# Optimization experiments

Hardware: AMD Instinct MI355X
Metric: run time of the kernel (lower is better)

The kernel has to match this reference:

```python
import jax, jax.numpy as jnp
import numpy as np

N_LEVELS = 16  # 3**16 = 43_046_721


def setup_inputs() -> dict:
    key = jax.random.key(0)
    k1, k2 = jax.random.split(key)
    f = jax.random.normal(k1, (3 ** N_LEVELS,), dtype=jnp.float32)
    # torch.rand -> uniform [0, 1)
    Phi_P = jax.random.uniform(k2, (N_LEVELS, 3, 3), dtype=jnp.float32)
    return {"f": f, "Phi_P": Phi_P}


def reference(f, Phi_P):
    N = Phi_P.shape[0]
    # Row-orthonormalize each 3x3 block: QR of Phi_P^T, then take Q^T
    Q, _ = jnp.linalg.qr(jnp.swapaxes(Phi_P, -2, -1))  # batched reduced QR
    Phi = jnp.swapaxes(Q, -2, -1)  # [N, 3, 3], orthonormal rows

    # Recursive Haar-style butterfly. At level i, f has length 3**(N-i).
    # Detail coefficients (rows j=1,2) land in slots [3**(N-i-1), 3**(N-i));
    # the row-0 (average) branch recurses. Build segments and concatenate
    # in reverse to avoid scatter into a preallocated buffer.
    segs = []
    for i in range(N):
        fm = f.reshape(-1, 3)            # [3**(N-i-1), 3]
        d1 = fm @ Phi[i, 1, :]           # detail j=1
        d2 = fm @ Phi[i, 2, :]           # detail j=2
        segs.append(jnp.concatenate([d1, d2]))
        f = fm @ Phi[i, 0, :]            # average branch, length /3
    # f now has length 1; its single entry is f_hat[0]
    f_hat = jnp.concatenate([f[:1]] + segs[::-1])
    return f_hat
```

## Files before the change

### kernel.cpp

```cpp
#include <hip/hip_runtime.h>

#define TPB 256

typedef float f32x4 __attribute__((ext_vector_type(4)));

__device__ __forceinline__ void block_sync_lds() {
    asm volatile("s_waitcnt lgkmcnt(0)" ::: "memory");
    __builtin_amdgcn_s_barrier();
    asm volatile("" ::: "memory");
}

__device__ __forceinline__ float sgpr(float x) {
    return __int_as_float(__builtin_amdgcn_readfirstlane(__float_as_int(x)));
}

__device__ __forceinline__ void gload_lds16(const float* g, float* l) {
    __builtin_amdgcn_global_load_lds(
        (const __attribute__((address_space(1))) void*)g,
        (__attribute__((address_space(3))) void*)l, 16, 0, 0);
}
__device__ __forceinline__ void gload_lds4(const float* g, float* l) {
    __builtin_amdgcn_global_load_lds(
        (const __attribute__((address_space(1))) void*)g,
        (__attribute__((address_space(3))) void*)l, 4, 0, 0);
}

__device__ __forceinline__ void qr3(const float* __restrict__ M, float* __restrict__ P) {
    float A[3][3];
#pragma unroll
    for (int r = 0; r < 3; ++r)
#pragma unroll
        for (int c = 0; c < 3; ++c)
            A[r][c] = M[c * 3 + r];

    float V[3][3], tau[3];
#pragma unroll
    for (int k = 0; k < 3; ++k) {
        float alpha = A[k][k];
        float xn2 = 0.f;
#pragma unroll
        for (int r = k + 1; r < 3; ++r) xn2 += A[r][k] * A[r][k];
        float t = 0.f;
        float v[3] = {0.f, 0.f, 0.f};
        v[k] = 1.f;
        if (xn2 > 0.f) {
            float beta = -copysignf(sqrtf(alpha * alpha + xn2), alpha);
            t = (beta - alpha) / beta;
            float inv = 1.f / (alpha - beta);
#pragma unroll
            for (int r = k + 1; r < 3; ++r) v[r] = A[r][k] * inv;
#pragma unroll
            for (int c = 0; c < 3; ++c) {
                if (c < k) continue;
                float w = 0.f;
#pragma unroll
                for (int r = 0; r < 3; ++r) if (r >= k) w += v[r] * A[r][c];
                w *= t;
#pragma unroll
                for (int r = 0; r < 3; ++r) if (r >= k) A[r][c] -= w * v[r];
            }
        }
        tau[k] = t;
#pragma unroll
        for (int r = 0; r < 3; ++r) V[k][r] = v[r];
    }
    float Q[3][3] = {{1.f, 0.f, 0.f}, {0.f, 1.f, 0.f}, {0.f, 0.f, 1.f}};
#pragma unroll
    for (int k = 2; k >= 0; --k) {
#pragma unroll
        for (int c = 0; c < 3; ++c) {
            float w = 0.f;
#pragma unroll
            for (int r = 0; r < 3; ++r) w += V[k][r] * Q[r][c];
            w *= tau[k];
#pragma unroll
            for (int r = 0; r < 3; ++r) Q[r][c] -= w * V[k][r];
        }
    }
#pragma unroll
    for (int r = 0; r < 3; ++r)
#pragma unroll
        for (int c = 0; c < 3; ++c)
            P[r * 3 + c] = Q[c][r];
}

#define ORG_D1L0 0
#define ORG_D2L0 1160
#define ORG_D1L1 2320
#define ORG_D2L1 2712
#define ORG_D1L2 3104
#define ORG_D2L2 3240

__global__ __launch_bounds__(TPB, 8) void fused3_kernel(
        const float* __restrict__ in, float* __restrict__ out,
        float* __restrict__ avg_out, const float* __restrict__ PhiP,
        int lvl, int m2) {
    __shared__ float s[3456];
    const int  t = threadIdx.x;
    const long b = blockIdx.x;
    const long nF = 27L * m2;
    const long fBase = 3456L * b;
    const long M0 = 9L * m2, M1 = 3L * m2, M2 = m2;

    const bool full = (128L * (b + 1) <= (long)m2);

    const long A0 = M0 + 1152L * b;
    const long A1 = 2 * M0 + 1152L * b;
    const long A2 = M1 + 384L * b;
    const long A3 = 2 * M1 + 384L * b;
    const long A4 = M2 + 128L * b;
    const long A5 = 2 * M2 + 128L * b;
    const int o0 = (int)(A0 & 3), o1 = (int)(A1 & 3), o2 = (int)(A2 & 3);
    const int o3 = (int)(A3 & 3), o4 = (int)(A4 & 3), o5 = (int)(A5 & 3);

    if (full) {
        const float* src = in + fBase;
#pragma unroll
        for (int r = 0; r < 3; ++r) {
            int c = 256 * r + t;
            gload_lds16(src + 4 * c, &s[4 * c]);
        }
        {
            int c = 608 + t;
            gload_lds16(src + 4 * c, &s[4 * c]);
        }
    } else {
        const long rem = nF - fBase;
        for (int i = t; i < 3456; i += TPB) s[i] = (i < rem) ? in[fBase + i] : 0.f;
    }

    float P[27];
    qr3(PhiP + 9L * lvl,       P + 0);
    qr3(PhiP + 9L * (lvl + 1), P + 9);
    qr3(PhiP + 9L * (lvl + 2), P + 18);
#pragma unroll
    for (int j = 0; j < 27; ++j) P[j] = sgpr(P[j]);

    __syncthreads();

    float f[27];
    const bool act = (t < 128);
    if (act) {
#pragma unroll
        for (int j = 0; j < 27; ++j) f[j] = s[27 * t + j];
    }
    block_sync_lds();

    float c;
    if (act) {
        float a[9];
#pragma unroll
        for (int g = 0; g < 9; ++g) {
            float x = f[3 * g], y = f[3 * g + 1], z = f[3 * g + 2];
            a[g] = x * P[0] + y * P[1] + z * P[2];
            s[ORG_D1L0 + o0 + 9 * t + g] = x * P[3] + y * P[4] + z * P[5];
            s[ORG_D2L0 + o1 + 9 * t + g] = x * P[6] + y * P[7] + z * P[8];
        }
        float bb[3];
#pragma unroll
        for (int h = 0; h < 3; ++h) {
            float x = a[3 * h], y = a[3 * h + 1], z = a[3 * h + 2];
            bb[h] = x * P[9] + y * P[10] + z * P[11];
            s[ORG_D1L1 + o2 + 3 * t + h] = x * P[12] + y * P[13] + z * P[14];
            s[ORG_D2L1 + o3 + 3 * t + h] = x * P[15] + y * P[16] + z * P[17];
        }
        float x = bb[0], y = bb[1], z = bb[2];
        c = x * P[18] + y * P[19] + z * P[20];
        s[ORG_D1L2 + o4 + t] = x * P[21] + y * P[22] + z * P[23];
        s[ORG_D2L2 + o5 + t] = x * P[24] + y * P[25] + z * P[26];
    }
    block_sync_lds();

#define STORE_SEC(ORG, A, O, CNT, ROUNDS)                                      \
    {                                                                          \
        float* dst = out + (A);                                                \
        const int aH = (4 - (O)) & 3;                                          \
        const int nb = ((CNT) - aH) >> 2;                                      \
        const int tl = (CNT) - aH - 4 * nb;                                    \
        if (t < aH) __builtin_nontemporal_store(s[(ORG) + (O) + t], dst + t);  \
        _Pragma("unroll")                                                      \
        for (int r = 0; r < (ROUNDS); ++r) {                                   \
            int idx = 256 * r + t;                                             \
            if (idx < nb) {                                                    \
                f32x4 vv = *reinterpret_cast<const f32x4*>(                    \
                    &s[(ORG) + (O) + aH + 4 * idx]);                           \
                __builtin_nontemporal_store(                                   \
                    vv, reinterpret_cast<f32x4*>(dst + aH) + idx);             \
            }                                                                  \
        }                                                                      \
        if (t < tl)                                                            \
            __builtin_nontemporal_store(s[(ORG) + (O) + aH + 4 * nb + t],      \
                                        dst + aH + 4 * nb + t);                \
    }

    if (full) {
        STORE_SEC(ORG_D1L0, A0, o0, 1152, 2);
        STORE_SEC(ORG_D2L0, A1, o1, 1152, 2);
        STORE_SEC(ORG_D1L1, A2, o2, 384, 1);
        STORE_SEC(ORG_D2L1, A3, o3, 384, 1);
        STORE_SEC(ORG_D1L2, A4, o4, 128, 1);
        STORE_SEC(ORG_D2L2, A5, o5, 128, 1);
        if (act) avg_out[128L * b + t] = c;
    } else {
#pragma unroll
        for (int r = 0; r < 5; ++r) {
            int i = 256 * r + t;
            long g = 1152L * b + i;
            if (i < 1152 && g < M0) {
                __builtin_nontemporal_store(s[ORG_D1L0 + o0 + i], out + M0 + g);
                __builtin_nontemporal_store(s[ORG_D2L0 + o1 + i], out + 2 * M0 + g);
            }
        }
#pragma unroll
        for (int r = 0; r < 2; ++r) {
            int i = 256 * r + t;
            long g = 384L * b + i;
            if (i < 384 && g < M1) {
                __builtin_nontemporal_store(s[ORG_D1L1 + o2 + i], out + M1 + g);
                __builtin_nontemporal_store(s[ORG_D2L1 + o3 + i], out + 2 * M1 + g);
            }
        }
        long g = 128L * b + t;
        if (act && g < M2) {
            __builtin_nontemporal_store(s[ORG_D1L2 + o4 + t], out + M2 + g);
            __builtin_nontemporal_store(s[ORG_D2L2 + o5 + t], out + 2 * M2 + g);
            avg_out[g] = c;
        }
    }
#undef STORE_SEC
}

__global__ __launch_bounds__(TPB) void mid_kernel(
        const float* __restrict__ in, float* __restrict__ out,
        float* __restrict__ avg_out, const float* __restrict__ PhiP) {
    __shared__ float s[6912];
    __shared__ float sc[243];
    __shared__ float sc2[81];
    __shared__ float sc3[27];
    __shared__ float sPhi[54];
    const int  t = threadIdx.x;
    const long b = blockIdx.x;
    const float* src = in + 6561L * b;

#pragma unroll
    for (int r = 0; r < 26; ++r) {
        int i = 256 * r + t;
        gload_lds4(src + i, &s[i]);
    }
    if (t < 6) {
        float P[9];
        qr3(PhiP + 9L * (3 + t), P);
#pragma unroll
        for (int j = 0; j < 9; ++j) sPhi[9 * t + j] = P[j];
    }
    __syncthreads();

    float P[27];
#pragma unroll
    for (int j = 0; j < 27; ++j) P[j] = sgpr(sPhi[j]);

    float f27[27];
    const bool act = (t < 243);
    if (act) {
#pragma unroll
        for (int j = 0; j < 27; ++j) f27[j] = s[27 * t + j];
    }
    block_sync_lds();

    if (act) {
        float a[9];
#pragma unroll
        for (int g = 0; g < 9; ++g) {
            float x = f27[3 * g], y = f27[3 * g + 1], z = f27[3 * g + 2];
            a[g] = x * P[0] + y * P[1] + z * P[2];
            s[9 * t + g]        = x * P[3] + y * P[4] + z * P[5];
            s[2187 + 9 * t + g] = x * P[6] + y * P[7] + z * P[8];
        }
        float bb[3];
#pragma unroll
        for (int h = 0; h < 3; ++h) {
            float x = a[3 * h], y = a[3 * h + 1], z = a[3 * h + 2];
            bb[h] = x * P[9] + y * P[10] + z * P[11];
            s[4374 + 3 * t + h] = x * P[12] + y * P[13] + z * P[14];
            s[5103 + 3 * t + h] = x * P[15] + y * P[16] + z * P[17];
        }
        float x = bb[0], y = bb[1], z = bb[2];
        sc[t]        = x * P[18] + y * P[19] + z * P[20];
        s[5832 + t]  = x * P[21] + y * P[22] + z * P[23];
        s[6075 + t]  = x * P[24] + y * P[25] + z * P[26];
    }
    block_sync_lds();

    if (t < 81) {
        float x = sc[3 * t], y = sc[3 * t + 1], z = sc[3 * t + 2];
        sc2[t]      = x * sPhi[27] + y * sPhi[28] + z * sPhi[29];
        s[6318 + t] = x * sPhi[30] + y * sPhi[31] + z * sPhi[32];
        s[6399 + t] = x * sPhi[33] + y * sPhi[34] + z * sPhi[35];
    }
    block_sync_lds();
    if (t < 27) {
        float x = sc2[3 * t], y = sc2[3 * t + 1], z = sc2[3 * t + 2];
        sc3[t]      = x * sPhi[36] + y * sPhi[37] + z * sPhi[38];
        s[6480 + t] = x * sPhi[39] + y * sPhi[40] + z * sPhi[41];
        s[6507 + t] = x * sPhi[42] + y * sPhi[43] + z * sPhi[44];
    }
    block_sync_lds();
    if (t < 9) {
        float x = sc3[3 * t], y = sc3[3 * t + 1], z = sc3[3 * t + 2];
        avg_out[9 * b + t] = x * sPhi[45] + y * sPhi[46] + z * sPhi[47];
        s[6534 + t] = x * sPhi[48] + y * sPhi[49] + z * sPhi[50];
        s[6543 + t] = x * sPhi[51] + y * sPhi[52] + z * sPhi[53];
    }
    block_sync_lds();

    const long B0 = 2187L * b, B1 = 729L * b, B2 = 243L * b;
    const long B3 = 81L * b, B4 = 27L * b, B5 = 9L * b;
#pragma unroll
    for (int r = 0; r < 9; ++r) {
        int i = 256 * r + t;
        if (i < 2187) {
            __builtin_nontemporal_store(s[i],        out + 531441 + B0 + i);
            __builtin_nontemporal_store(s[2187 + i], out + 2 * 531441 + B0 + i);
        }
    }
#pragma unroll
    for (int r = 0; r < 3; ++r) {
        int i = 256 * r + t;
        if (i < 729) {
            __builtin_nontemporal_store(s[4374 + i], out + 177147 + B1 + i);
            __builtin_nontemporal_store(s[5103 + i], out + 2 * 177147 + B1 + i);
        }
    }
    if (t < 243) {
        __builtin_nontemporal_store(s[5832 + t], out + 59049 + B2 + t);
        __builtin_nontemporal_store(s[6075 + t], out + 2 * 59049 + B2 + t);
    }
    if (t < 81) {
        __builtin_nontemporal_store(s[6318 + t], out + 19683 + B3 + t);
        __builtin_nontemporal_store(s[6399 + t], out + 2 * 19683 + B3 + t);
    }
    if (t < 27) {
        __builtin_nontemporal_store(s[6480 + t], out + 6561 + B4 + t);
        __builtin_nontemporal_store(s[6507 + t], out + 2 * 6561 + B4 + t);
    }
    if (t < 9) {
        __builtin_nontemporal_store(s[6534 + t], out + 2187 + B5 + t);
        __builtin_nontemporal_store(s[6543 + t], out + 2 * 2187 + B5 + t);
    }
}

#define TTPB 1024
__global__ __launch_bounds__(TTPB) void tail_kernel(
        const float* __restrict__ in, float* __restrict__ out,
        const float* __restrict__ PhiP) {
    __shared__ float s0[2187];
    __shared__ float s1[729];
    __shared__ float sPhi[63];
    const int lt = threadIdx.x;

    for (int i = lt; i < 2187; i += TTPB) s0[i] = in[i];
    if (lt < 7) {
        float P[9];
        qr3(PhiP + 9L * (9 + lt), P);
#pragma unroll
        for (int j = 0; j < 9; ++j) sPhi[lt * 9 + j] = P[j];
    }
    __syncthreads();

    float* cur = s0;
    float* nxt = s1;
    int len = 2187;
#pragma unroll
    for (int L = 0; L < 7; ++L) {
        int m = len / 3;
        float p0 = sPhi[L * 9 + 0], p1 = sPhi[L * 9 + 1], p2 = sPhi[L * 9 + 2];
        float q0 = sPhi[L * 9 + 3], q1 = sPhi[L * 9 + 4], q2 = sPhi[L * 9 + 5];
        float r0 = sPhi[L * 9 + 6], r1 = sPhi[L * 9 + 7], r2 = sPhi[L * 9 + 8];
        for (int t = lt; t < m; t += TTPB) {
            float x = cur[3 * t], y = cur[3 * t + 1], z = cur[3 * t + 2];
            out[m + t]     = x * q0 + y * q1 + z * q2;
            out[2 * m + t] = x * r0 + y * r1 + z * r2;
            nxt[t]         = x * p0 + y * p1 + z * p2;
        }
        block_sync_lds();
        float* tmp = cur; cur = nxt; nxt = tmp;
        len = m;
    }
    if (lt == 0) out[0] = cur[0];
}

extern "C" void kernel_launch(void* const* d_in, const int* in_sizes, int n_in,
                              void* d_out, int out_size, void* d_ws, size_t ws_size,
                              hipStream_t stream) {
    const float* f    = (const float*)d_in[0];
    const float* PhiP = (const float*)d_in[1];
    float* out = (float*)d_out;
    float* ws  = (float*)d_ws;

    float* bufA = ws;
    float* bufC = bufA + 1594323;

    const int m2_0 = 1594323;
    const int grid1 = (m2_0 + 127) / 128;
    fused3_kernel<<<grid1, TPB, 0, stream>>>(f, out, bufA, PhiP, 0, m2_0);

    mid_kernel<<<243, TPB, 0, stream>>>(bufA, out, bufC, PhiP);

    tail_kernel<<<1, TTPB, 0, stream>>>(bufC, out, PhiP);
}
```

Measured before the change: 69.52 us.

## Fuse tail kernel into mid kernel via last-block atomic counter

Removes the separate single-block tail launch. Each mid_kernel block now bumps a global atomic counter, and the last block to finish runs the remaining seven levels on bufC using its shared memory. This saves one kernel launch and its gap, at the cost of a memset, a threadfence in every block, and running the tail with 256 threads instead of 1024.

```diff
diff --git a/kernel.cpp b/kernel.cpp
--- a/kernel.cpp
+++ b/kernel.cpp
@@ -232,12 +232,14 @@
 
 __global__ __launch_bounds__(TPB) void mid_kernel(
         const float* __restrict__ in, float* __restrict__ out,
-        float* __restrict__ avg_out, const float* __restrict__ PhiP) {
+        float* __restrict__ bufC, const float* __restrict__ PhiP,
+        int* __restrict__ cnt) {
     __shared__ float s[6912];
     __shared__ float sc[243];
     __shared__ float sc2[81];
     __shared__ float sc3[27];
-    __shared__ float sPhi[54];
+    __shared__ float sPhi[117];
+    __shared__ int sLast;
     const int  t = threadIdx.x;
     const long b = blockIdx.x;
     const float* src = in + 6561L * b;
@@ -247,7 +249,7 @@
         int i = 256 * r + t;
         gload_lds4(src + i, &s[i]);
     }
-    if (t < 6) {
+    if (t < 13) {
         float P[9];
         qr3(PhiP + 9L * (3 + t), P);
 #pragma unroll
@@ -307,7 +309,7 @@
     block_sync_lds();
     if (t < 9) {
         float x = sc3[3 * t], y = sc3[3 * t + 1], z = sc3[3 * t + 2];
-        avg_out[9 * b + t] = x * sPhi[45] + y * sPhi[46] + z * sPhi[47];
+        bufC[9 * b + t] = x * sPhi[45] + y * sPhi[46] + z * sPhi[47];
         s[6534 + t] = x * sPhi[48] + y * sPhi[49] + z * sPhi[50];
         s[6543 + t] = x * sPhi[51] + y * sPhi[52] + z * sPhi[53];
     }
@@ -347,46 +349,42 @@
         __builtin_nontemporal_store(s[6534 + t], out + 2187 + B5 + t);
         __builtin_nontemporal_store(s[6543 + t], out + 2 * 2187 + B5 + t);
     }
-}
-
-#define TTPB 1024
-__global__ __launch_bounds__(TTPB) void tail_kernel(
-        const float* __restrict__ in, float* __restrict__ out,
-        const float* __restrict__ PhiP) {
-    __shared__ float s0[2187];
-    __shared__ float s1[729];
-    __shared__ float sPhi[63];
-    const int lt = threadIdx.x;
-
-    for (int i = lt; i < 2187; i += TTPB) s0[i] = in[i];
-    if (lt < 7) {
-        float P[9];
-        qr3(PhiP + 9L * (9 + lt), P);
-#pragma unroll
-        for (int j = 0; j < 9; ++j) sPhi[lt * 9 + j] = P[j];
-    }
+
+    __threadfence();
     __syncthreads();
-
-    float* cur = s0;
-    float* nxt = s1;
+    if (t == 0) {
+        int old = __hip_atomic_fetch_add(cnt, 1, __ATOMIC_ACQ_REL,
+                                         __HIP_MEMORY_SCOPE_AGENT);
+        sLast = (old == 242);
+    }
+    __syncthreads();
+    if (!sLast) return;
+
+    __threadfence();
+    block_sync_lds();
+    for (int i = t; i < 2187; i += TPB) s[i] = bufC[i];
+    block_sync_lds();
+
+    float* cur = s;
+    float* nxt = s + 2187;
     int len = 2187;
 #pragma unroll
     for (int L = 0; L < 7; ++L) {
         int m = len / 3;
-        float p0 = sPhi[L * 9 + 0], p1 = sPhi[L * 9 + 1], p2 = sPhi[L * 9 + 2];
-        float q0 = sPhi[L * 9 + 3], q1 = sPhi[L * 9 + 4], q2 = sPhi[L * 9 + 5];
-        float r0 = sPhi[L * 9 + 6], r1 = sPhi[L * 9 + 7], r2 = sPhi[L * 9 + 8];
-        for (int t = lt; t < m; t += TTPB) {
-            float x = cur[3 * t], y = cur[3 * t + 1], z = cur[3 * t + 2];
-            out[m + t]     = x * q0 + y * q1 + z * q2;
-            out[2 * m + t] = x * r0 + y * r1 + z * r2;
-            nxt[t]         = x * p0 + y * p1 + z * p2;
+        float p0 = sPhi[54 + L * 9 + 0], p1 = sPhi[54 + L * 9 + 1], p2 = sPhi[54 + L * 9 + 2];
+        float q0 = sPhi[54 + L * 9 + 3], q1 = sPhi[54 + L * 9 + 4], q2 = sPhi[54 + L * 9 + 5];
+        float r0 = sPhi[54 + L * 9 + 6], r1 = sPhi[54 + L * 9 + 7], r2 = sPhi[54 + L * 9 + 8];
+        for (int u = t; u < m; u += TPB) {
+            float x = cur[3 * u], y = cur[3 * u + 1], z = cur[3 * u + 2];
+            out[m + u]     = x * q0 + y * q1 + z * q2;
+            out[2 * m + u] = x * r0 + y * r1 + z * r2;
+            nxt[u]         = x * p0 + y * p1 + z * p2;
         }
         block_sync_lds();
         float* tmp = cur; cur = nxt; nxt = tmp;
         len = m;
     }
-    if (lt == 0) out[0] = cur[0];
+    if (t == 0) out[0] = cur[0];
 }
 
 extern "C" void kernel_launch(void* const* d_in, const int* in_sizes, int n_in,
@@ -399,12 +397,13 @@
 
     float* bufA = ws;
     float* bufC = bufA + 1594323;
+    int*   cnt  = (int*)(bufC + 2188);
+
+    hipMemsetAsync(cnt, 0, sizeof(int), stream);
 
     const int m2_0 = 1594323;
     const int grid1 = (m2_0 + 127) / 128;
     fused3_kernel<<<grid1, TPB, 0, stream>>>(f, out, bufA, PhiP, 0, m2_0);
 
-    mid_kernel<<<243, TPB, 0, stream>>>(bufA, out, bufC, PhiP);
-
-    tail_kernel<<<1, TTPB, 0, stream>>>(bufC, out, PhiP);
-}
+    mid_kernel<<<243, TPB, 0, stream>>>(bufA, out, bufC, PhiP, cnt);
+}
```

New measurement: 101.7 us. 1.46x slower.
